# Optimization experiments

Measured on AMD Instinct MI355X. Metric: run time of the kernel, lower is better.

The kernel has to match this reference:

```python
import jax, jax.numpy as jnp
import numpy as np

B, T, D = 2, 2048, 1024
H = 16
HD = D // H  # 64


def setup_inputs() -> dict:
    key = jax.random.key(0)
    k1, k2, k3, k4, k5 = jax.random.split(key, 5)
    s = 0.02
    return {
        "x": jax.random.normal(k1, (B, T, D), dtype=jnp.float32),
        "Wqkv": jax.random.normal(k2, (D, 3 * D), dtype=jnp.float32) * s,
        "bqkv": jax.random.normal(k3, (3 * D,), dtype=jnp.float32) * s,
        "Wout": jax.random.normal(k4, (D, D), dtype=jnp.float32) * s,
        "bout": jax.random.normal(k5, (D,), dtype=jnp.float32) * s,
    }


def reference(x, Wqkv, bqkv, Wout, bout):
    b, t, c = x.shape
    qkv = (x @ Wqkv + bqkv).reshape(b, t, 3, H, HD)
    q = jnp.transpose(qkv[:, :, 0], (0, 2, 1, 3))  # [B,H,T,HD]
    k = jnp.transpose(qkv[:, :, 1], (0, 2, 1, 3))
    v = jnp.transpose(qkv[:, :, 2], (0, 2, 1, 3))
    att = jnp.einsum("bhqd,bhkd->bhqk", q, k) * (HD ** -0.5)
    mask = jnp.tril(jnp.ones((t, t), dtype=bool))  # causal, no past kv
    att = jnp.where(mask, att, -jnp.inf)
    att = jax.nn.softmax(att, axis=-1)
    y = jnp.einsum("bhqk,bhkd->bhqd", att, v)
    y = jnp.transpose(y, (0, 2, 1, 3)).reshape(b, t, c)
    return y @ Wout + bout
```

## Files before the change

kernel.cpp:

```cpp
#include <hip/hip_runtime.h>
#include <hip/hip_bf16.h>
#include <math.h>

#define B_  2
#define T_  2048
#define D_  1024
#define H_  16
#define HD_ 64

typedef __attribute__((ext_vector_type(8))) short short8;
typedef __attribute__((ext_vector_type(4))) float f32x4;

#if __has_builtin(__builtin_amdgcn_exp2f)
#define EXP2F __builtin_amdgcn_exp2f
#else
#define EXP2F exp2f
#endif

__device__ __forceinline__ ushort f2bf(float x) {
    unsigned u = __builtin_bit_cast(unsigned, x);
    return (ushort)((u + 0x7FFFu + ((u >> 16) & 1u)) >> 16);
}

__device__ __forceinline__ unsigned pack_bf2_fast(float a, float b) {
    unsigned ua = __builtin_bit_cast(unsigned, a) + 0x8000u;
    unsigned ub = __builtin_bit_cast(unsigned, b) + 0x8000u;
    return (ua >> 16) | (ub & 0xFFFF0000u);
}

__device__ __forceinline__ void load_lds_16B(const ushort* g, ushort* l) {
    __builtin_amdgcn_global_load_lds(
        (const __attribute__((address_space(1))) unsigned*)g,
        (__attribute__((address_space(3))) unsigned*)l, 16, 0, 0);
}

__global__ __launch_bounds__(256)
void prep_kernel(const float* __restrict__ x, ushort* __restrict__ xb,
                 const float* __restrict__ Wqkv, ushort* __restrict__ Wqkvt,
                 const float* __restrict__ Wout, ushort* __restrict__ Woutt)
{
    __shared__ ushort Ts[64][65];
    const int bid = blockIdx.x;

    if (bid < 512) {
        const int n4 = (B_ * T_ * D_) / 4;
        for (int i = bid * 256 + threadIdx.x; i < n4; i += 512 * 256) {
            float4 v = ((const float4*)x)[i];
            ushort4 o = { f2bf(v.x), f2bf(v.y), f2bf(v.z), f2bf(v.w) };
            ((ushort4*)xb)[i] = o;
        }
        return;
    }

    const float* W; ushort* Wt; int K, M, m0, k0;
    if (bid < 1280) {
        const int t = bid - 512;
        W = Wqkv; Wt = Wqkvt; K = D_; M = 3 * D_;
        m0 = (t % 48) * 64; k0 = (t / 48) * 64;
    } else {
        const int t = bid - 1280;
        W = Wout; Wt = Woutt; K = D_; M = D_;
        m0 = (t % 16) * 64; k0 = (t / 16) * 64;
    }

    const int tr = threadIdx.x >> 4;
    const int tc = threadIdx.x & 15;
    #pragma unroll
    for (int it = 0; it < 4; it++) {
        int k = tr + it * 16;
        float4 v = *(const float4*)&W[(size_t)(k0 + k) * M + m0 + tc * 4];
        Ts[tc * 4 + 0][k] = f2bf(v.x);
        Ts[tc * 4 + 1][k] = f2bf(v.y);
        Ts[tc * 4 + 2][k] = f2bf(v.z);
        Ts[tc * 4 + 3][k] = f2bf(v.w);
    }
    __syncthreads();
    #pragma unroll
    for (int it = 0; it < 2; it++) {
        const int mr  = (threadIdx.x >> 3) + it * 32;
        const int seg = (threadIdx.x & 7) * 8;
        short8 v;
        #pragma unroll
        for (int r = 0; r < 8; r++) v[r] = (short)Ts[mr][seg + r];
        *(short8*)&Wt[(size_t)(m0 + mr) * K + k0 + seg] = v;
    }
}

__global__ __launch_bounds__(256, 4)
void gemm_qkv(const ushort* __restrict__ A, const ushort* __restrict__ Bt,
              const float* __restrict__ bias,
              ushort* __restrict__ Qg, ushort* __restrict__ Kg,
              ushort* __restrict__ Vtg)
{
    const int K = D_;
    __shared__ __align__(16) ushort lds[16384];
    ushort* Asl = lds;
    ushort* Bsl = lds + 8192;

    const int tid = threadIdx.x;
    const int w  = tid >> 6, L = tid & 63;
    const int lt = L & 15, lq = L >> 4;
    const int wr = w >> 1, wc = w & 1;
    const int m0 = blockIdx.x * 128, n0 = blockIdx.y * 128;
    const int rsub = L >> 3;
    const int pgr  = L & 7;

    f32x4 acc[4][4] = {};

    for (int k0 = 0; k0 < K; k0 += 64) {
        __syncthreads();
        #pragma unroll
        for (int j = 0; j < 4; j++) {
            const int row  = (w * 4 + j) * 8 + rsub;
            const int gran = pgr ^ rsub;
            load_lds_16B(A  + (size_t)(n0 + row) * K + k0 + gran * 8,
                         &Asl[row * 64 + pgr * 8]);
            load_lds_16B(Bt + (size_t)(m0 + row) * K + k0 + gran * 8,
                         &Bsl[row * 64 + pgr * 8]);
        }
        __syncthreads();

        #pragma unroll
        for (int ks = 0; ks < 2; ks++) {
            short8 af[4], bf[4];
            #pragma unroll
            for (int i = 0; i < 4; i++) {
                const int ra = wr * 64 + i * 16 + lt;
                af[i] = *(const short8*)&Asl[ra * 64 + (((ks * 4 + lq) ^ (ra & 7)) * 8)];
                const int rb = wc * 64 + i * 16 + lt;
                bf[i] = *(const short8*)&Bsl[rb * 64 + (((ks * 4 + lq) ^ (rb & 7)) * 8)];
            }
            #pragma unroll
            for (int i = 0; i < 4; i++)
                #pragma unroll
                for (int j = 0; j < 4; j++)
                    acc[i][j] = __builtin_amdgcn_mfma_f32_16x16x32_bf16(af[i], bf[j], acc[i][j], 0, 0, 0);
        }
    }

    __syncthreads();
    const int s  = m0 >> 10;
    const int h0 = (m0 & 1023) >> 6;
    const float qs = (s == 0) ? 0.18033688011112042f : 1.0f;

    if (s < 2) {
        #pragma unroll
        for (int j = 0; j < 4; j++) {
            const int m  = wc * 64 + j * 16 + lt;
            const float bv = bias[m0 + m];
            #pragma unroll
            for (int i = 0; i < 4; i++) {
                const int n = wr * 64 + i * 16 + lq * 4;
                #pragma unroll
                for (int r = 0; r < 4; r++)
                    lds[(n + r) * 128 + m] = f2bf((acc[i][j][r] + bv) * qs);
            }
        }
        __syncthreads();
        ushort* dst = (s == 0 ? Qg : Kg);
        #pragma unroll
        for (int it = 0; it < 8; it++) {
            const int g   = tid + it * 256;
            const int row = g >> 4, c = g & 15;
            const int n = n0 + row;
            const int b = n >> 11, t = n & 2047;
            const int h = h0 + (c >> 3), d = (c & 7) * 8;
            short8 v = *(const short8*)&lds[row * 128 + c * 8];
            *(short8*)&dst[((size_t)(b * H_ + h) * T_ + t) * HD_ + d] = v;
        }
    } else {
        #pragma unroll
        for (int j = 0; j < 4; j++) {
            const int m  = wc * 64 + j * 16 + lt;
            const float bv = bias[m0 + m];
            #pragma unroll
            for (int i = 0; i < 4; i++) {
                const int n = wr * 64 + i * 16 + lq * 4;
                uint2 pk = { pack_bf2_fast(acc[i][j][0] + bv, acc[i][j][1] + bv),
                             pack_bf2_fast(acc[i][j][2] + bv, acc[i][j][3] + bv) };
                *(uint2*)&lds[m * 128 + n] = pk;
            }
        }
        __syncthreads();
        const int b = n0 >> 11, t0 = n0 & 2047;
        #pragma unroll
        for (int it = 0; it < 8; it++) {
            const int g   = tid + it * 256;
            const int row = g >> 4, c = g & 15;
            const int h = h0 + (row >> 6), d = row & 63;
            short8 v = *(const short8*)&lds[row * 128 + c * 8];
            *(short8*)&Vtg[((size_t)(b * H_ + h) * HD_ + d) * T_ + t0 + c * 8] = v;
        }
    }
}

__global__ __launch_bounds__(256, 4)
void gemm_out(const ushort* __restrict__ A, const ushort* __restrict__ Bt,
              const float* __restrict__ bias, float* __restrict__ C)
{
    const int K = D_, M = D_;
    __shared__ __align__(16) ushort lds[8192 + 4096];
    ushort* Asl = lds;
    ushort* Bsl = lds + 8192;

    const int tid = threadIdx.x;
    const int w  = tid >> 6, L = tid & 63;
    const int lt = L & 15, lq = L >> 4;
    const int wr = w >> 1, wc = w & 1;
    const int m0 = blockIdx.x * 64, n0 = blockIdx.y * 128;
    const int rsub = L >> 3;
    const int pgr  = L & 7;

    f32x4 acc[2][4] = {};

    for (int k0 = 0; k0 < K; k0 += 64) {
        __syncthreads();
        #pragma unroll
        for (int j = 0; j < 4; j++) {
            const int row  = (w * 4 + j) * 8 + rsub;
            const int gran = pgr ^ rsub;
            load_lds_16B(A + (size_t)(n0 + row) * K + k0 + gran * 8,
                         &Asl[row * 64 + pgr * 8]);
        }
        #pragma unroll
        for (int j = 0; j < 2; j++) {
            const int row  = (w * 2 + j) * 8 + rsub;
            const int gran = pgr ^ rsub;
            load_lds_16B(Bt + (size_t)(m0 + row) * K + k0 + gran * 8,
                         &Bsl[row * 64 + pgr * 8]);
        }
        __syncthreads();

        #pragma unroll
        for (int ks = 0; ks < 2; ks++) {
            short8 wf[2], yf[4];
            #pragma unroll
            for (int j = 0; j < 2; j++) {
                const int rb = wc * 32 + j * 16 + lt;
                wf[j] = *(const short8*)&Bsl[rb * 64 + (((ks * 4 + lq) ^ (rb & 7)) * 8)];
            }
            #pragma unroll
            for (int i = 0; i < 4; i++) {
                const int ra = wr * 64 + i * 16 + lt;
                yf[i] = *(const short8*)&Asl[ra * 64 + (((ks * 4 + lq) ^ (ra & 7)) * 8)];
            }
            #pragma unroll
            for (int j = 0; j < 2; j++)
                #pragma unroll
                for (int i = 0; i < 4; i++)
                    acc[j][i] = __builtin_amdgcn_mfma_f32_16x16x32_bf16(wf[j], yf[i], acc[j][i], 0, 0, 0);
        }
    }

    #pragma unroll
    for (int j = 0; j < 2; j++) {
        const int mbase = m0 + wc * 32 + j * 16 + lq * 4;
        const float4 bv = *(const float4*)&bias[mbase];
        #pragma unroll
        for (int i = 0; i < 4; i++) {
            const int n = n0 + wr * 64 + i * 16 + lt;
            float4 o = { acc[j][i][0] + bv.x, acc[j][i][1] + bv.y,
                         acc[j][i][2] + bv.z, acc[j][i][3] + bv.w };
            *(float4*)&C[(size_t)n * M + mbase] = o;
        }
    }
}

__global__ __launch_bounds__(256, 2)
void attn_mfma(const ushort* __restrict__ Qg, const ushort* __restrict__ Kg,
               const ushort* __restrict__ Vtg, ushort* __restrict__ yb)
{
    const int h = blockIdx.y, b = blockIdx.z;
    const int flip = ((blockIdx.y >> 3) ^ blockIdx.z) & 1;
    const int qb = flip ? blockIdx.x : (15 - blockIdx.x);
    const int tid = threadIdx.x;
    const int w  = tid >> 6, L = tid & 63;
    const int lt = L & 15, lq = L >> 4;
    const int kswz = lt & 7;

    __shared__ __align__(16) ushort Ks [128 * 64];
    __shared__ __align__(16) ushort Vts[64 * 128];
    __shared__ __align__(16) ushort Ps [4][2][16 * 40];

    const size_t bh = (size_t)(b * H_ + h);
    const ushort* Qbase  = Qg  + bh * T_ * HD_;
    const ushort* Kbase  = Kg  + bh * T_ * HD_;
    const ushort* Vtbase = Vtg + bh * HD_ * T_;

    const int q0 = qb * 128 + w * 16 + lt;
    const int q1 = q0 + 64;
    const short8 qf00 = *(const short8*)(Qbase + (size_t)q0 * HD_ + lq * 8);
    const short8 qf01 = *(const short8*)(Qbase + (size_t)q0 * HD_ + 32 + lq * 8);
    const short8 qf10 = *(const short8*)(Qbase + (size_t)q1 * HD_ + lq * 8);
    const short8 qf11 = *(const short8*)(Qbase + (size_t)q1 * HD_ + 32 + lq * 8);

    f32x4 acc0[4] = {}, acc1[4] = {};
    float lsum0 = 0.f, lsum1 = 0.f;

    const int krow = tid >> 3, kpg = tid & 7;
    const int vrow = tid >> 4, vpg = tid & 15;

    for (int kb = 0; kb <= qb; kb++) {
        __syncthreads();
        #pragma unroll
        for (int rr = 0; rr < 4; rr++) {
            const int row = krow + 32 * rr;
            load_lds_16B(Kbase + (size_t)(kb * 128 + row) * HD_ + (kpg ^ (row & 7)) * 8,
                         &Ks[row * 64 + kpg * 8]);
        }
        #pragma unroll
        for (int rr = 0; rr < 4; rr++) {
            const int d = vrow + 16 * rr;
            load_lds_16B(Vtbase + (size_t)d * T_ + kb * 128 + (vpg ^ (d & 7)) * 8,
                         &Vts[d * 128 + vpg * 8]);
        }
        __syncthreads();

        const bool lastkb = (kb == qb);
        #pragma unroll
        for (int ks = 0; ks < 4; ks++) {
            const int row0 = (2 * ks) * 16 + lt;
            const int row1 = row0 + 16;
            short8 a00 = *(const short8*)&Ks[row0 * 64 + ((lq ^ kswz) * 8)];
            short8 a01 = *(const short8*)&Ks[row0 * 64 + (((4 + lq) ^ kswz) * 8)];
            short8 a10 = *(const short8*)&Ks[row1 * 64 + ((lq ^ kswz) * 8)];
            short8 a11 = *(const short8*)&Ks[row1 * 64 + (((4 + lq) ^ kswz) * 8)];
            f32x4 c00 = {}, c01 = {}, c10 = {}, c11 = {};
            __builtin_amdgcn_s_setprio(1);
            c00 = __builtin_amdgcn_mfma_f32_16x16x32_bf16(a00, qf00, c00, 0, 0, 0);
            c00 = __builtin_amdgcn_mfma_f32_16x16x32_bf16(a01, qf01, c00, 0, 0, 0);
            c01 = __builtin_amdgcn_mfma_f32_16x16x32_bf16(a10, qf00, c01, 0, 0, 0);
            c01 = __builtin_amdgcn_mfma_f32_16x16x32_bf16(a11, qf01, c01, 0, 0, 0);
            c10 = __builtin_amdgcn_mfma_f32_16x16x32_bf16(a00, qf10, c10, 0, 0, 0);
            c10 = __builtin_amdgcn_mfma_f32_16x16x32_bf16(a01, qf11, c10, 0, 0, 0);
            c11 = __builtin_amdgcn_mfma_f32_16x16x32_bf16(a10, qf10, c11, 0, 0, 0);
            c11 = __builtin_amdgcn_mfma_f32_16x16x32_bf16(a11, qf11, c11, 0, 0, 0);
            __builtin_amdgcn_s_setprio(0);

            float p0[8], p1[8];
            #pragma unroll
            for (int r = 0; r < 4; r++) {
                p0[r]     = EXP2F(c00[r]);
                p0[4 + r] = EXP2F(c01[r]);
                p1[r]     = EXP2F(c10[r]);
                p1[4 + r] = EXP2F(c11[r]);
            }
            if (lastkb) {
                const int key0 = kb * 128 + (2 * ks) * 16 + lq * 4;
                #pragma unroll
                for (int r = 0; r < 4; r++) {
                    if (key0 + r > q0)      p0[r]     = 0.f;
                    if (key0 + 16 + r > q0) p0[4 + r] = 0.f;
                    if (key0 + r > q1)      p1[r]     = 0.f;
                    if (key0 + 16 + r > q1) p1[4 + r] = 0.f;
                }
            }
            lsum0 += ((p0[0] + p0[1]) + (p0[2] + p0[3])) + ((p0[4] + p0[5]) + (p0[6] + p0[7]));
            lsum1 += ((p1[0] + p1[1]) + (p1[2] + p1[3])) + ((p1[4] + p1[5]) + (p1[6] + p1[7]));
            uint2 pk00 = { pack_bf2_fast(p0[0], p0[1]), pack_bf2_fast(p0[2], p0[3]) };
            uint2 pk01 = { pack_bf2_fast(p0[4], p0[5]), pack_bf2_fast(p0[6], p0[7]) };
            uint2 pk10 = { pack_bf2_fast(p1[0], p1[1]), pack_bf2_fast(p1[2], p1[3]) };
            uint2 pk11 = { pack_bf2_fast(p1[4], p1[5]), pack_bf2_fast(p1[6], p1[7]) };
            *(uint2*)&Ps[w][0][lt * 40 + lq * 4]      = pk00;
            *(uint2*)&Ps[w][0][lt * 40 + 16 + lq * 4] = pk01;
            *(uint2*)&Ps[w][1][lt * 40 + lq * 4]      = pk10;
            *(uint2*)&Ps[w][1][lt * 40 + 16 + lq * 4] = pk11;

            short8 pf0 = *(const short8*)&Ps[w][0][lt * 40 + lq * 8];
            short8 pf1 = *(const short8*)&Ps[w][1][lt * 40 + lq * 8];

            __builtin_amdgcn_s_setprio(1);
            #pragma unroll
            for (int dt = 0; dt < 4; dt++) {
                const int vr = dt * 16 + lt;
                short8 vf = *(const short8*)&Vts[vr * 128 + (((ks * 4 + lq) ^ kswz) * 8)];
                acc0[dt] = __builtin_amdgcn_mfma_f32_16x16x32_bf16(pf0, vf, acc0[dt], 0, 0, 0);
                acc1[dt] = __builtin_amdgcn_mfma_f32_16x16x32_bf16(pf1, vf, acc1[dt], 0, 0, 0);
            }
            __builtin_amdgcn_s_setprio(0);
        }
    }

    lsum0 += __shfl_xor(lsum0, 16, 64);
    lsum0 += __shfl_xor(lsum0, 32, 64);
    lsum1 += __shfl_xor(lsum1, 16, 64);
    lsum1 += __shfl_xor(lsum1, 32, 64);
    const float inv0 = 1.0f / lsum0;
    const float inv1 = 1.0f / lsum1;

    float linv0[4], linv1[4];
    #pragma unroll
    for (int r = 0; r < 4; r++) {
        linv0[r] = __shfl(inv0, lq * 4 + r, 64);
        linv1[r] = __shfl(inv1, lq * 4 + r, 64);
    }

    ushort* y0 = yb + (size_t)(b * T_ + qb * 128 + w * 16) * D_ + h * HD_;
    ushort* y1 = y0 + (size_t)64 * D_;
    #pragma unroll
    for (int r = 0; r < 4; r++)
        #pragma unroll
        for (int dt = 0; dt < 4; dt++) {
            y0[(size_t)(lq * 4 + r) * D_ + dt * 16 + lt] = f2bf(acc0[dt][r] * linv0[r]);
            y1[(size_t)(lq * 4 + r) * D_ + dt * 16 + lt] = f2bf(acc1[dt][r] * linv1[r]);
        }
}

extern "C" void kernel_launch(void* const* d_in, const int* in_sizes, int n_in,
                              void* d_out, int out_size, void* d_ws, size_t ws_size,
                              hipStream_t stream)
{
    const float* x    = (const float*)d_in[0];
    const float* Wqkv = (const float*)d_in[1];
    const float* bqkv = (const float*)d_in[2];
    const float* Wout = (const float*)d_in[3];
    const float* bout = (const float*)d_in[4];
    float* out = (float*)d_out;

    char* ws = (char*)d_ws;
    const size_t NT = (size_t)B_ * T_;
    ushort* xb     = (ushort*)ws;
    ushort* Wqkvt  = (ushort*)(ws + NT * D_ * 2);
    ushort* Woutt  = (ushort*)(ws + NT * D_ * 2 + (size_t)3 * D_ * D_ * 2);
    char*   p      = ws + NT * D_ * 2 + (size_t)4 * D_ * D_ * 2;
    const size_t qkv_elems = (size_t)B_ * H_ * T_ * HD_;
    ushort* Qg  = (ushort*)p;
    ushort* Kg  = (ushort*)(p + qkv_elems * 2);
    ushort* Vtg = (ushort*)(p + qkv_elems * 4);
    ushort* yb  = (ushort*)(p + qkv_elems * 6);

    prep_kernel<<<1536, 256, 0, stream>>>(x, xb, Wqkv, Wqkvt, Wout, Woutt);

    gemm_qkv<<<dim3(3 * D_ / 128, NT / 128), 256, 0, stream>>>(
        xb, Wqkvt, bqkv, Qg, Kg, Vtg);

    attn_mfma<<<dim3(16, H_, B_), 256, 0, stream>>>(Qg, Kg, Vtg, yb);

    gemm_out<<<dim3(D_ / 64, NT / 128), 256, 0, stream>>>(
        yb, Woutt, bout, out);
}
```

Measured before the change: 176.0 us.

## Double-buffer K/V tiles in LDS to overlap loads with attention compute

Attention K and V^T tiles are now held in two LDS buffers. The next key block is issued as an async load-to-LDS before computing the current one, with a partial vmcnt wait so only the current stage's loads are awaited. This hides global-memory latency behind the MFMA and softmax work. In exchange LDS usage roughly doubles, which may pressure occupancy, and correctness relies on the manual wait counts matching the load instructions.

```diff
diff --git a/kernel.cpp b/kernel.cpp
--- a/kernel.cpp
+++ b/kernel.cpp
@@ -278,8 +278,8 @@
     const int lt = L & 15, lq = L >> 4;
     const int kswz = lt & 7;
 
-    __shared__ __align__(16) ushort Ks [128 * 64];
-    __shared__ __align__(16) ushort Vts[64 * 128];
+    __shared__ __align__(16) ushort Ks [2][128 * 64];
+    __shared__ __align__(16) ushort Vts[2][64 * 128];
     __shared__ __align__(16) ushort Ps [4][2][16 * 40];
 
     const size_t bh = (size_t)(b * H_ + h);
@@ -300,31 +300,47 @@
     const int krow = tid >> 3, kpg = tid & 7;
     const int vrow = tid >> 4, vpg = tid & 15;
 
-    for (int kb = 0; kb <= qb; kb++) {
-        __syncthreads();
+    auto STAGE = [&](int kb, int buf) {
+        ushort* KsD  = &Ks [buf][0];
+        ushort* VtsD = &Vts[buf][0];
         #pragma unroll
         for (int rr = 0; rr < 4; rr++) {
             const int row = krow + 32 * rr;
             load_lds_16B(Kbase + (size_t)(kb * 128 + row) * HD_ + (kpg ^ (row & 7)) * 8,
-                         &Ks[row * 64 + kpg * 8]);
+                         &KsD[row * 64 + kpg * 8]);
         }
         #pragma unroll
         for (int rr = 0; rr < 4; rr++) {
             const int d = vrow + 16 * rr;
             load_lds_16B(Vtbase + (size_t)d * T_ + kb * 128 + (vpg ^ (d & 7)) * 8,
-                         &Vts[d * 128 + vpg * 8]);
-        }
-        __syncthreads();
-
+                         &VtsD[d * 128 + vpg * 8]);
+        }
+    };
+
+    STAGE(0, 0);
+    int cur = 0;
+
+    for (int kb = 0; kb <= qb; kb++) {
+        if (kb < qb) {
+            STAGE(kb + 1, cur ^ 1);
+            asm volatile("s_waitcnt vmcnt(8)" ::: "memory");
+        } else {
+            asm volatile("s_waitcnt vmcnt(0)" ::: "memory");
+        }
+        __builtin_amdgcn_s_barrier();
+        __builtin_amdgcn_sched_barrier(0);
+
+        const ushort* Ksc  = &Ks [cur][0];
+        const ushort* Vtsc = &Vts[cur][0];
         const bool lastkb = (kb == qb);
         #pragma unroll
         for (int ks = 0; ks < 4; ks++) {
             const int row0 = (2 * ks) * 16 + lt;
             const int row1 = row0 + 16;
-            short8 a00 = *(const short8*)&Ks[row0 * 64 + ((lq ^ kswz) * 8)];
-            short8 a01 = *(const short8*)&Ks[row0 * 64 + (((4 + lq) ^ kswz) * 8)];
-            short8 a10 = *(const short8*)&Ks[row1 * 64 + ((lq ^ kswz) * 8)];
-            short8 a11 = *(const short8*)&Ks[row1 * 64 + (((4 + lq) ^ kswz) * 8)];
+            short8 a00 = *(const short8*)&Ksc[row0 * 64 + ((lq ^ kswz) * 8)];
+            short8 a01 = *(const short8*)&Ksc[row0 * 64 + (((4 + lq) ^ kswz) * 8)];
+            short8 a10 = *(const short8*)&Ksc[row1 * 64 + ((lq ^ kswz) * 8)];
+            short8 a11 = *(const short8*)&Ksc[row1 * 64 + (((4 + lq) ^ kswz) * 8)];
             f32x4 c00 = {}, c01 = {}, c10 = {}, c11 = {};
             __builtin_amdgcn_s_setprio(1);
             c00 = __builtin_amdgcn_mfma_f32_16x16x32_bf16(a00, qf00, c00, 0, 0, 0);
@@ -373,12 +389,15 @@
             #pragma unroll
             for (int dt = 0; dt < 4; dt++) {
                 const int vr = dt * 16 + lt;
-                short8 vf = *(const short8*)&Vts[vr * 128 + (((ks * 4 + lq) ^ kswz) * 8)];
+                short8 vf = *(const short8*)&Vtsc[vr * 128 + (((ks * 4 + lq) ^ kswz) * 8)];
                 acc0[dt] = __builtin_amdgcn_mfma_f32_16x16x32_bf16(pf0, vf, acc0[dt], 0, 0, 0);
                 acc1[dt] = __builtin_amdgcn_mfma_f32_16x16x32_bf16(pf1, vf, acc1[dt], 0, 0, 0);
             }
             __builtin_amdgcn_s_setprio(0);
         }
+
+        __builtin_amdgcn_s_barrier();
+        cur ^= 1;
     }
 
     lsum0 += __shfl_xor(lsum0, 16, 64);
```

New measurement: 174.8 us. No clear change (-0.7%).

## Shrink attention query tiles to 64 rows and keep P in registers

Applied to the files above, without the earlier changes.

The attention kernel now uses 64-query blocks of 2 waves (128 threads) with twice as many blocks, which gives finer causal load balancing and more blocks for scheduling. The K rows are permuted with a new swizzle so the QK^T MFMA output layout lines up with the PV A-operand layout. That lets P be packed directly in registers instead of round-tripping through LDS. The diagonal tile handles half-tiles by skipping key subtiles, and the setprio hints are dropped. Each block still loads full 128-key K/V tiles, so LDS traffic per query roughly doubles.

```diff
diff --git a/kernel.cpp b/kernel.cpp
--- a/kernel.cpp
+++ b/kernel.cpp
@@ -10,6 +10,7 @@
 
 typedef __attribute__((ext_vector_type(8))) short short8;
 typedef __attribute__((ext_vector_type(4))) float f32x4;
+typedef __attribute__((ext_vector_type(4))) unsigned uint32x4;
 
 #if __has_builtin(__builtin_amdgcn_exp2f)
 #define EXP2F __builtin_amdgcn_exp2f
@@ -266,13 +267,13 @@
     }
 }
 
-__global__ __launch_bounds__(256, 2)
+__global__ __launch_bounds__(128, 2)
 void attn_mfma(const ushort* __restrict__ Qg, const ushort* __restrict__ Kg,
                const ushort* __restrict__ Vtg, ushort* __restrict__ yb)
 {
     const int h = blockIdx.y, b = blockIdx.z;
     const int flip = ((blockIdx.y >> 3) ^ blockIdx.z) & 1;
-    const int qb = flip ? blockIdx.x : (15 - blockIdx.x);
+    const int qb = flip ? blockIdx.x : (31 - blockIdx.x);
     const int tid = threadIdx.x;
     const int w  = tid >> 6, L = tid & 63;
     const int lt = L & 15, lq = L >> 4;
@@ -280,15 +281,14 @@
 
     __shared__ __align__(16) ushort Ks [128 * 64];
     __shared__ __align__(16) ushort Vts[64 * 128];
-    __shared__ __align__(16) ushort Ps [4][2][16 * 40];
 
     const size_t bh = (size_t)(b * H_ + h);
     const ushort* Qbase  = Qg  + bh * T_ * HD_;
     const ushort* Kbase  = Kg  + bh * T_ * HD_;
     const ushort* Vtbase = Vtg + bh * HD_ * T_;
 
-    const int q0 = qb * 128 + w * 16 + lt;
-    const int q1 = q0 + 64;
+    const int q0 = qb * 64 + w * 32 + lt;
+    const int q1 = q0 + 16;
     const short8 qf00 = *(const short8*)(Qbase + (size_t)q0 * HD_ + lq * 8);
     const short8 qf01 = *(const short8*)(Qbase + (size_t)q0 * HD_ + 32 + lq * 8);
     const short8 qf10 = *(const short8*)(Qbase + (size_t)q1 * HD_ + lq * 8);
@@ -299,85 +299,128 @@
 
     const int krow = tid >> 3, kpg = tid & 7;
     const int vrow = tid >> 4, vpg = tid & 15;
-
-    for (int kb = 0; kb <= qb; kb++) {
-        __syncthreads();
-        #pragma unroll
-        for (int rr = 0; rr < 4; rr++) {
-            const int row = krow + 32 * rr;
-            load_lds_16B(Kbase + (size_t)(kb * 128 + row) * HD_ + (kpg ^ (row & 7)) * 8,
+    const int nk = (qb + 2) >> 1;
+
+    const int prow = ((lt >> 2) * 8) + (lt & 3);
+
+    for (int kb = 0; kb < nk; kb++) {
+        __syncthreads();
+        #pragma unroll
+        for (int rr = 0; rr < 8; rr++) {
+            const int row = krow + 16 * rr;
+            const int swzK = (((row >> 3) & 1) * 4) | (row & 3);
+            load_lds_16B(Kbase + (size_t)(kb * 128 + row) * HD_ + (kpg ^ swzK) * 8,
                          &Ks[row * 64 + kpg * 8]);
         }
         #pragma unroll
-        for (int rr = 0; rr < 4; rr++) {
-            const int d = vrow + 16 * rr;
+        for (int rr = 0; rr < 8; rr++) {
+            const int d = vrow + 8 * rr;
             load_lds_16B(Vtbase + (size_t)d * T_ + kb * 128 + (vpg ^ (d & 7)) * 8,
                          &Vts[d * 128 + vpg * 8]);
         }
         __syncthreads();
 
-        const bool lastkb = (kb == qb);
-        #pragma unroll
-        for (int ks = 0; ks < 4; ks++) {
-            const int row0 = (2 * ks) * 16 + lt;
-            const int row1 = row0 + 16;
-            short8 a00 = *(const short8*)&Ks[row0 * 64 + ((lq ^ kswz) * 8)];
-            short8 a01 = *(const short8*)&Ks[row0 * 64 + (((4 + lq) ^ kswz) * 8)];
-            short8 a10 = *(const short8*)&Ks[row1 * 64 + ((lq ^ kswz) * 8)];
-            short8 a11 = *(const short8*)&Ks[row1 * 64 + (((4 + lq) ^ kswz) * 8)];
-            f32x4 c00 = {}, c01 = {}, c10 = {}, c11 = {};
-            __builtin_amdgcn_s_setprio(1);
-            c00 = __builtin_amdgcn_mfma_f32_16x16x32_bf16(a00, qf00, c00, 0, 0, 0);
-            c00 = __builtin_amdgcn_mfma_f32_16x16x32_bf16(a01, qf01, c00, 0, 0, 0);
-            c01 = __builtin_amdgcn_mfma_f32_16x16x32_bf16(a10, qf00, c01, 0, 0, 0);
-            c01 = __builtin_amdgcn_mfma_f32_16x16x32_bf16(a11, qf01, c01, 0, 0, 0);
-            c10 = __builtin_amdgcn_mfma_f32_16x16x32_bf16(a00, qf10, c10, 0, 0, 0);
-            c10 = __builtin_amdgcn_mfma_f32_16x16x32_bf16(a01, qf11, c10, 0, 0, 0);
-            c11 = __builtin_amdgcn_mfma_f32_16x16x32_bf16(a10, qf10, c11, 0, 0, 0);
-            c11 = __builtin_amdgcn_mfma_f32_16x16x32_bf16(a11, qf11, c11, 0, 0, 0);
-            __builtin_amdgcn_s_setprio(0);
-
-            float p0[8], p1[8];
-            #pragma unroll
-            for (int r = 0; r < 4; r++) {
-                p0[r]     = EXP2F(c00[r]);
-                p0[4 + r] = EXP2F(c01[r]);
-                p1[r]     = EXP2F(c10[r]);
-                p1[4 + r] = EXP2F(c11[r]);
-            }
-            if (lastkb) {
-                const int key0 = kb * 128 + (2 * ks) * 16 + lq * 4;
+        if (kb < nk - 1) {
+            #pragma unroll
+            for (int ks = 0; ks < 4; ks++) {
+                const int row0 = ks * 32 + prow;
+                const int row1 = row0 + 4;
+                short8 a00 = *(const short8*)&Ks[row0 * 64 + ((lq ^ kswz) * 8)];
+                short8 a01 = *(const short8*)&Ks[row0 * 64 + (((4 + lq) ^ kswz) * 8)];
+                short8 a10 = *(const short8*)&Ks[row1 * 64 + ((lq ^ kswz) * 8)];
+                short8 a11 = *(const short8*)&Ks[row1 * 64 + (((4 + lq) ^ kswz) * 8)];
+                f32x4 c00 = {}, c01 = {}, c10 = {}, c11 = {};
+                c00 = __builtin_amdgcn_mfma_f32_16x16x32_bf16(a00, qf00, c00, 0, 0, 0);
+                c00 = __builtin_amdgcn_mfma_f32_16x16x32_bf16(a01, qf01, c00, 0, 0, 0);
+                c01 = __builtin_amdgcn_mfma_f32_16x16x32_bf16(a10, qf00, c01, 0, 0, 0);
+                c01 = __builtin_amdgcn_mfma_f32_16x16x32_bf16(a11, qf01, c01, 0, 0, 0);
+                c10 = __builtin_amdgcn_mfma_f32_16x16x32_bf16(a00, qf10, c10, 0, 0, 0);
+                c10 = __builtin_amdgcn_mfma_f32_16x16x32_bf16(a01, qf11, c10, 0, 0, 0);
+                c11 = __builtin_amdgcn_mfma_f32_16x16x32_bf16(a10, qf10, c11, 0, 0, 0);
+                c11 = __builtin_amdgcn_mfma_f32_16x16x32_bf16(a11, qf11, c11, 0, 0, 0);
+
+                float p0[8], p1[8];
                 #pragma unroll
                 for (int r = 0; r < 4; r++) {
-                    if (key0 + r > q0)      p0[r]     = 0.f;
-                    if (key0 + 16 + r > q0) p0[4 + r] = 0.f;
-                    if (key0 + r > q1)      p1[r]     = 0.f;
-                    if (key0 + 16 + r > q1) p1[4 + r] = 0.f;
+                    p0[r]     = EXP2F(c00[r]);
+                    p0[4 + r] = EXP2F(c01[r]);
+                    p1[r]     = EXP2F(c10[r]);
+                    p1[4 + r] = EXP2F(c11[r]);
                 }
-            }
-            lsum0 += ((p0[0] + p0[1]) + (p0[2] + p0[3])) + ((p0[4] + p0[5]) + (p0[6] + p0[7]));
-            lsum1 += ((p1[0] + p1[1]) + (p1[2] + p1[3])) + ((p1[4] + p1[5]) + (p1[6] + p1[7]));
-            uint2 pk00 = { pack_bf2_fast(p0[0], p0[1]), pack_bf2_fast(p0[2], p0[3]) };
-            uint2 pk01 = { pack_bf2_fast(p0[4], p0[5]), pack_bf2_fast(p0[6], p0[7]) };
-            uint2 pk10 = { pack_bf2_fast(p1[0], p1[1]), pack_bf2_fast(p1[2], p1[3]) };
-            uint2 pk11 = { pack_bf2_fast(p1[4], p1[5]), pack_bf2_fast(p1[6], p1[7]) };
-            *(uint2*)&Ps[w][0][lt * 40 + lq * 4]      = pk00;
-            *(uint2*)&Ps[w][0][lt * 40 + 16 + lq * 4] = pk01;
-            *(uint2*)&Ps[w][1][lt * 40 + lq * 4]      = pk10;
-            *(uint2*)&Ps[w][1][lt * 40 + 16 + lq * 4] = pk11;
-
-            short8 pf0 = *(const short8*)&Ps[w][0][lt * 40 + lq * 8];
-            short8 pf1 = *(const short8*)&Ps[w][1][lt * 40 + lq * 8];
-
-            __builtin_amdgcn_s_setprio(1);
-            #pragma unroll
-            for (int dt = 0; dt < 4; dt++) {
-                const int vr = dt * 16 + lt;
-                short8 vf = *(const short8*)&Vts[vr * 128 + (((ks * 4 + lq) ^ kswz) * 8)];
-                acc0[dt] = __builtin_amdgcn_mfma_f32_16x16x32_bf16(pf0, vf, acc0[dt], 0, 0, 0);
-                acc1[dt] = __builtin_amdgcn_mfma_f32_16x16x32_bf16(pf1, vf, acc1[dt], 0, 0, 0);
-            }
-            __builtin_amdgcn_s_setprio(0);
+                lsum0 += ((p0[0] + p0[1]) + (p0[2] + p0[3])) + ((p0[4] + p0[5]) + (p0[6] + p0[7]));
+                lsum1 += ((p1[0] + p1[1]) + (p1[2] + p1[3])) + ((p1[4] + p1[5]) + (p1[6] + p1[7]));
+
+                uint32x4 pw0 = { pack_bf2_fast(p0[0], p0[1]), pack_bf2_fast(p0[2], p0[3]),
+                                 pack_bf2_fast(p0[4], p0[5]), pack_bf2_fast(p0[6], p0[7]) };
+                uint32x4 pw1 = { pack_bf2_fast(p1[0], p1[1]), pack_bf2_fast(p1[2], p1[3]),
+                                 pack_bf2_fast(p1[4], p1[5]), pack_bf2_fast(p1[6], p1[7]) };
+                short8 pf0 = __builtin_bit_cast(short8, pw0);
+                short8 pf1 = __builtin_bit_cast(short8, pw1);
+
+                #pragma unroll
+                for (int dt = 0; dt < 4; dt++) {
+                    const int vr = dt * 16 + lt;
+                    short8 vf = *(const short8*)&Vts[vr * 128 + (((ks * 4 + lq) ^ kswz) * 8)];
+                    acc0[dt] = __builtin_amdgcn_mfma_f32_16x16x32_bf16(pf0, vf, acc0[dt], 0, 0, 0);
+                    acc1[dt] = __builtin_amdgcn_mfma_f32_16x16x32_bf16(pf1, vf, acc1[dt], 0, 0, 0);
+                }
+            }
+        } else {
+            const int ksN = (qb & 1) ? 4 : 2;
+            const int mk0 = (qb & 1) ? 2 : 0;
+            for (int ks = 0; ks < ksN; ks++) {
+                const int row0 = ks * 32 + prow;
+                const int row1 = row0 + 4;
+                short8 a00 = *(const short8*)&Ks[row0 * 64 + ((lq ^ kswz) * 8)];
+                short8 a01 = *(const short8*)&Ks[row0 * 64 + (((4 + lq) ^ kswz) * 8)];
+                short8 a10 = *(const short8*)&Ks[row1 * 64 + ((lq ^ kswz) * 8)];
+                short8 a11 = *(const short8*)&Ks[row1 * 64 + (((4 + lq) ^ kswz) * 8)];
+                f32x4 c00 = {}, c01 = {}, c10 = {}, c11 = {};
+                c00 = __builtin_amdgcn_mfma_f32_16x16x32_bf16(a00, qf00, c00, 0, 0, 0);
+                c00 = __builtin_amdgcn_mfma_f32_16x16x32_bf16(a01, qf01, c00, 0, 0, 0);
+                c01 = __builtin_amdgcn_mfma_f32_16x16x32_bf16(a10, qf00, c01, 0, 0, 0);
+                c01 = __builtin_amdgcn_mfma_f32_16x16x32_bf16(a11, qf01, c01, 0, 0, 0);
+                c10 = __builtin_amdgcn_mfma_f32_16x16x32_bf16(a00, qf10, c10, 0, 0, 0);
+                c10 = __builtin_amdgcn_mfma_f32_16x16x32_bf16(a01, qf11, c10, 0, 0, 0);
+                c11 = __builtin_amdgcn_mfma_f32_16x16x32_bf16(a10, qf10, c11, 0, 0, 0);
+                c11 = __builtin_amdgcn_mfma_f32_16x16x32_bf16(a11, qf11, c11, 0, 0, 0);
+
+                float p0[8], p1[8];
+                #pragma unroll
+                for (int r = 0; r < 4; r++) {
+                    p0[r]     = EXP2F(c00[r]);
+                    p0[4 + r] = EXP2F(c01[r]);
+                    p1[r]     = EXP2F(c10[r]);
+                    p1[4 + r] = EXP2F(c11[r]);
+                }
+                if (ks >= mk0) {
+                    const int key0 = kb * 128 + ks * 32 + lq * 8;
+                    #pragma unroll
+                    for (int r = 0; r < 4; r++) {
+                        if (key0 + r > q0)     p0[r]     = 0.f;
+                        if (key0 + 4 + r > q0) p0[4 + r] = 0.f;
+                        if (key0 + r > q1)     p1[r]     = 0.f;
+                        if (key0 + 4 + r > q1) p1[4 + r] = 0.f;
+                    }
+                }
+                lsum0 += ((p0[0] + p0[1]) + (p0[2] + p0[3])) + ((p0[4] + p0[5]) + (p0[6] + p0[7]));
+                lsum1 += ((p1[0] + p1[1]) + (p1[2] + p1[3])) + ((p1[4] + p1[5]) + (p1[6] + p1[7]));
+
+                uint32x4 pw0 = { pack_bf2_fast(p0[0], p0[1]), pack_bf2_fast(p0[2], p0[3]),
+                                 pack_bf2_fast(p0[4], p0[5]), pack_bf2_fast(p0[6], p0[7]) };
+                uint32x4 pw1 = { pack_bf2_fast(p1[0], p1[1]), pack_bf2_fast(p1[2], p1[3]),
+                                 pack_bf2_fast(p1[4], p1[5]), pack_bf2_fast(p1[6], p1[7]) };
+                short8 pf0 = __builtin_bit_cast(short8, pw0);
+                short8 pf1 = __builtin_bit_cast(short8, pw1);
+
+                #pragma unroll
+                for (int dt = 0; dt < 4; dt++) {
+                    const int vr = dt * 16 + lt;
+                    short8 vf = *(const short8*)&Vts[vr * 128 + (((ks * 4 + lq) ^ kswz) * 8)];
+                    acc0[dt] = __builtin_amdgcn_mfma_f32_16x16x32_bf16(pf0, vf, acc0[dt], 0, 0, 0);
+                    acc1[dt] = __builtin_amdgcn_mfma_f32_16x16x32_bf16(pf1, vf, acc1[dt], 0, 0, 0);
+                }
+            }
         }
     }
 
@@ -395,8 +438,8 @@
         linv1[r] = __shfl(inv1, lq * 4 + r, 64);
     }
 
-    ushort* y0 = yb + (size_t)(b * T_ + qb * 128 + w * 16) * D_ + h * HD_;
-    ushort* y1 = y0 + (size_t)64 * D_;
+    ushort* y0 = yb + (size_t)(b * T_ + qb * 64 + w * 32) * D_ + h * HD_;
+    ushort* y1 = y0 + (size_t)16 * D_;
     #pragma unroll
     for (int r = 0; r < 4; r++)
         #pragma unroll
@@ -434,7 +477,7 @@
     gemm_qkv<<<dim3(3 * D_ / 128, NT / 128), 256, 0, stream>>>(
         xb, Wqkvt, bqkv, Qg, Kg, Vtg);
 
-    attn_mfma<<<dim3(16, H_, B_), 256, 0, stream>>>(Qg, Kg, Vtg, yb);
+    attn_mfma<<<dim3(32, H_, B_), 128, 0, stream>>>(Qg, Kg, Vtg, yb);
 
     gemm_out<<<dim3(D_ / 64, NT / 128), 256, 0, stream>>>(
         yb, Woutt, bout, out);
```

Result: no change. 178.1 us (+1.2%).
